# Optimization experiments

Hardware: AMD Instinct MI355X
Metric: run time of the kernel (lower is better)

Reference implementation:

```python
import jax, jax.numpy as jnp
import numpy as np

N, E, H, G, L = 50000, 640000, 128, 8, 3

def setup_inputs() -> dict:
    key = jax.random.key(0)
    ks = jax.random.split(key, 10)
    s = 1.0 / np.sqrt(H)
    return {
        "x": jax.random.normal(ks[0], (N, H), jnp.float32),
        "query": jax.random.normal(ks[1], (G, H), jnp.float32),
        "Wl": jax.random.normal(ks[2], (L, H, H), jnp.float32) * s,
        "bl": jax.random.normal(ks[3], (L, H), jnp.float32) * s,
        "Wr": jax.random.normal(ks[4], (L, H, H), jnp.float32) * s,
        "Wlin": jax.random.normal(ks[5], (H, H), jnp.float32) * s,
        "blin": jax.random.normal(ks[6], (H,), jnp.float32) * s,
        "edge_index": jax.random.randint(ks[7], (2, E), 0, N, jnp.int64),
        "batch_vec": jnp.sort(jax.random.randint(ks[8], (N,), 0, G, jnp.int64)),
    }

def reference(x, query, Wl, bl, Wr, Wlin, blin, edge_index, batch_vec):
    src, dst = edge_index[0], edge_index[1]
    n = x.shape[0]
    for i in range(L):
        # SAGEConv(aggr='max'): gather neighbor feats, scatter-max to dst
        m = jax.ops.segment_max(x[src], dst, num_segments=n)  # [N,H]
        m = jnp.where(jnp.isfinite(m), m, 0.0)  # isolated nodes -> 0 (PyG)
        x = jax.nn.relu(m @ Wl[i].T + bl[i] + x @ Wr[i].T)
    x = x @ Wlin.T + blin  # encoder final linear
    # cosine scoring per graph, vectorized via batch_vec
    xn = x / jnp.linalg.norm(x, axis=1, keepdims=True).clip(1e-12)
    qn = query / jnp.linalg.norm(query, axis=1, keepdims=True).clip(1e-12)
    scores = jnp.sum(xn * qn[batch_vec], axis=1)  # [N]
    return scores
```

## Files before the change

kernel.cpp:

```cpp
#include <hip/hip_runtime.h>
#include <math.h>

#define H 128

typedef _Float16 half8 __attribute__((ext_vector_type(8)));
typedef float f32x16 __attribute__((ext_vector_type(16)));
typedef int int4v __attribute__((ext_vector_type(4)));

__device__ __forceinline__ half8 h8max(half8 a, half8 b) {
#if defined(__has_builtin) && __has_builtin(__builtin_elementwise_max)
    return __builtin_elementwise_max(a, b);
#else
    half8 r;
#pragma unroll
    for (int j = 0; j < 8; ++j) r[j] = a[j] > b[j] ? a[j] : b[j];
    return r;
#endif
}

__device__ __forceinline__ half8 h8shfl_xor(half8 v, int mask) {
    int4v iv;
    __builtin_memcpy(&iv, &v, 16);
#pragma unroll
    for (int j = 0; j < 4; ++j) iv[j] = __shfl_xor(iv[j], mask, 64);
    half8 r;
    __builtin_memcpy(&r, &iv, 16);
    return r;
}


__global__ __launch_bounds__(256) void prep_all(
    const int* __restrict__ ei, int E, int* __restrict__ deg,
    int* __restrict__ govf, int* __restrict__ ovf, int* __restrict__ adjp32,
    const float* __restrict__ x, const float* __restrict__ query,
    const float* __restrict__ Wl, const float* __restrict__ Wr,
    const float* __restrict__ Wlin, _Float16* __restrict__ xh,
    _Float16* __restrict__ wimg, float* __restrict__ qn, int n8, int HB, int SB,
    int WB) {
    int b = blockIdx.x;
    int tid = threadIdx.x;
    if (b < HB) {
        int base = b * 2048 + tid;
        int sv[8], dv[8], posv[8];
#pragma unroll
        for (int k = 0; k < 8; ++k) {
            int e = base + k * 256;
            sv[k] = (e < E) ? ei[e] : 0;
            dv[k] = (e < E) ? ei[E + e] : -1;
        }
#pragma unroll
        for (int k = 0; k < 8; ++k)
            posv[k] = (dv[k] >= 0) ? atomicAdd(&deg[dv[k]], 1) : 0;
#pragma unroll
        for (int k = 0; k < 8; ++k) {
            if (dv[k] >= 0) {
                if (posv[k] < 32) {
                    adjp32[(size_t)dv[k] * 32 + posv[k]] = sv[k];
                } else {
                    int o = atomicAdd(govf, 1);
                    ovf[2 * o] = dv[k];
                    ovf[2 * o + 1] = sv[k];
                }
            }
        }
    } else if (b < HB + SB) {
        int i = (b - HB) * 256 + tid;
        if (i < n8) {
            const float4* x4 = (const float4*)x;
            float4 u = x4[(size_t)i * 2], v = x4[(size_t)i * 2 + 1];
            float f[8] = {u.x, u.y, u.z, u.w, v.x, v.y, v.z, v.w};
            half8 h;
#pragma unroll
            for (int j = 0; j < 8; ++j) h[j] = (_Float16)f[j];
            *(half8*)(xh + (size_t)i * 8) = h;
        }
    } else if (b < HB + SB + WB) {
        int gidx = (b - HB - SB) * 256 + tid;
        if (gidx < 7 * 2048) {
            int mat = gidx / 2048;
            int rem = gidx - mat * 2048;
            int kc4 = rem >> 9;
            int r2 = rem & 511;
            int s = r2 >> 6;
            int lane = r2 & 63;
            int ks = s >> 2;
            int colgrp = s & 3;
            int lhi = lane >> 5, l31 = lane & 31;
            int n = colgrp * 32 + l31;
            int g16 = kc4 * 4 + ks * 2 + lhi;
            const float* src = (mat == 6) ? Wlin
                             : ((mat & 1) ? Wr + (mat >> 1) * H * H
                                          : Wl + (mat >> 1) * H * H);
            const float* p = src + n * H + g16 * 8;
            half8 h, l;
#pragma unroll
            for (int j = 0; j < 8; ++j) {
                float v = p[j];
                _Float16 hh = (_Float16)v;
                h[j] = hh;
                l[j] = (_Float16)(v - (float)hh);
            }
            size_t base = (size_t)mat * 32768 + (size_t)kc4 * 8192 +
                          (size_t)s * 1024 + (size_t)lane * 16;
            *(half8*)(wimg + base) = h;
            *(half8*)(wimg + base + 8) = l;
        }
    } else {
        int g = b - HB - SB - WB;
        __shared__ float part[4];
        float v = (tid < 128) ? query[g * H + tid] : 0.f;
        float ss = v * v;
#pragma unroll
        for (int off = 32; off > 0; off >>= 1) ss += __shfl_xor(ss, off, 64);
        if ((tid & 63) == 0) part[tid >> 6] = ss;
        __syncthreads();
        float tot = part[0] + part[1];
        if (tid < 128) qn[g * H + tid] = v / fmaxf(sqrtf(tot), 1e-12f);
    }
}


template <bool FINAL_UNUSED>
__global__ __launch_bounds__(512, 8) void layer_fused(
    const half8* __restrict__ Xh, const int* __restrict__ deg,
    const int* __restrict__ adjp32, const int* __restrict__ ovf,
    const int* __restrict__ ovfcnt, const _Float16* __restrict__ Bimg,
    const float* __restrict__ bias, _Float16* __restrict__ Yh, int N) {
    __shared__ __align__(16) unsigned char smem[16384];
    _Float16* sU = (_Float16*)smem;
    _Float16* sX = (_Float16*)(smem + 8192);
    float* comb = (float*)smem;

    int tid = threadIdx.x;
    int w = tid >> 6;
    int wq = w & 3;
    int wh = w >> 2;
    int lane = tid & 63;
    int l31 = lane & 31;
    int lhi = lane >> 5;
    int n0 = blockIdx.x * 32;

    const half8 hz = {(_Float16)0.f, (_Float16)0.f, (_Float16)0.f, (_Float16)0.f,
                      (_Float16)0.f, (_Float16)0.f, (_Float16)0.f, (_Float16)0.f};

    {
        int row = tid >> 4;
        int g = tid & 15;
        int nn = n0 + row;
        half8 h = hz;
        if (nn < N) h = Xh[(size_t)nn * 16 + g];
        *(half8*)&sX[row * 128 + ((g ^ (row & 15)) << 3)] = h;
    }

    {
        int sub = lane >> 4;
        int lf = lane & 15;
        int nd4 = n0 + w * 4;
        int node = nd4 + sub;
        int nodec = node < N ? node : N - 1;
        int degv = (node < N) ? deg[node] : 0;

        int dmx = degv;
        {
            int t = __shfl_xor(dmx, 16, 64);
            dmx = t > dmx ? t : dmx;
            t = __shfl_xor(dmx, 32, 64);
            dmx = t > dmx ? t : dmx;
        }

        int r0 = adjp32[(size_t)nodec * 32 + lf];
        int r1 = 0;
        if (dmx > 16) r1 = adjp32[(size_t)nodec * 32 + 16 + lf];
#pragma unroll
        for (int i = 0; i < 4; ++i) {
            int d = __shfl(degv, i << 4, 64);
            int base = i << 4;
            int j0 = sub, j1 = 4 + sub, j2 = 8 + sub, j3 = 12 + sub;
            int i0 = __shfl(r0, base | (j0 < d ? j0 : 0), 64);
            int i1 = __shfl(r0, base | (j1 < d ? j1 : 0), 64);
            int i2 = __shfl(r0, base | (j2 < d ? j2 : 0), 64);
            int i3 = __shfl(r0, base | (j3 < d ? j3 : 0), 64);
            half8 v0 = Xh[(size_t)i0 * 16 + lf];
            half8 v1 = Xh[(size_t)i1 * 16 + lf];
            half8 v2 = Xh[(size_t)i2 * 16 + lf];
            half8 v3 = Xh[(size_t)i3 * 16 + lf];
            half8 acc = h8max(h8max(v0, v1), h8max(v2, v3));
            if (d > 16) {
                int k4 = (16 + sub) < d ? sub : 0;
                int k5 = (20 + sub) < d ? 4 + sub : 0;
                int k6 = (24 + sub) < d ? 8 + sub : 0;
                int k7 = (28 + sub) < d ? 12 + sub : 0;
                int i4 = __shfl(r1, base | k4, 64);
                int i5 = __shfl(r1, base | k5, 64);
                int i6 = __shfl(r1, base | k6, 64);
                int i7 = __shfl(r1, base | k7, 64);
                half8 u0 = Xh[(size_t)i4 * 16 + lf];
                half8 u1 = Xh[(size_t)i5 * 16 + lf];
                half8 u2 = Xh[(size_t)i6 * 16 + lf];
                half8 u3 = Xh[(size_t)i7 * 16 + lf];
                acc = h8max(acc, h8max(h8max(u0, u1), h8max(u2, u3)));
            }
            if (d > 32) {
                int cnt = ovfcnt[0];
                for (int k = 0; k < cnt; ++k) {
                    if (ovf[2 * k] == nd4 + i) {
                        half8 u = Xh[(size_t)ovf[2 * k + 1] * 16 + lf];
                        acc = h8max(acc, u);
                    }
                }
            }
            acc = h8max(acc, h8shfl_xor(acc, 16));
            acc = h8max(acc, h8shfl_xor(acc, 32));
            if (d == 0) acc = hz;
            int row = w * 4 + i;
            if (sub == 0) *(half8*)&sU[row * 128 + ((lf ^ (row & 15)) << 3)] = acc;
        }
    }
    __syncthreads();

    f32x16 acc;
    int col = wq * 32 + l31;
    {
        float b0 = (wh == 0) ? bias[col] : 0.f;
#pragma unroll
        for (int r = 0; r < 16; ++r) acc[r] = b0;
    }

    int rl = l31;
    const _Float16* A = wh ? sX : sU;
    const _Float16* B = Bimg + (size_t)wh * 32768;

#pragma unroll
    for (int kc4 = 0; kc4 < 4; ++kc4) {
#pragma unroll
        for (int ks = 0; ks < 2; ++ks) {
            int g16 = kc4 * 4 + ks * 2 + lhi;
            int posA = g16 ^ (rl & 15);
            half8 ah = *(const half8*)&A[rl * 128 + posA * 8];
            size_t boff =
                (size_t)kc4 * 8192 + (size_t)(ks * 4 + wq) * 1024 + (size_t)lane * 16;
            half8 bh = *(const half8*)&B[boff];
            half8 bl2 = *(const half8*)&B[boff + 8];
            acc = __builtin_amdgcn_mfma_f32_32x32x16_f16(ah, bh, acc, 0, 0, 0);
            acc = __builtin_amdgcn_mfma_f32_32x32x16_f16(ah, bl2, acc, 0, 0, 0);
        }
    }

    __syncthreads();

    if (wh == 1) {
#pragma unroll
        for (int r = 0; r < 16; ++r) {
            int rloc = (r & 3) + 8 * (r >> 2) + 4 * lhi;
            comb[wq * 1024 + rloc * 32 + l31] = acc[r];
        }
    }
    __syncthreads();

    if (wh == 0) {
#pragma unroll
        for (int r = 0; r < 16; ++r) {
            int rloc = (r & 3) + 8 * (r >> 2) + 4 * lhi;
            float y = acc[r] + comb[wq * 1024 + rloc * 32 + l31];
            int row = n0 + rloc;
            if (row < N) Yh[(size_t)row * H + col] = (_Float16)fmaxf(y, 0.f);
        }
    }
}


__global__ __launch_bounds__(256) void final_mfma6(
    const half8* __restrict__ Xh, const _Float16* __restrict__ Bimg,
    const float* __restrict__ blin, const float* __restrict__ qn,
    const int* __restrict__ bv, float* __restrict__ out, int N) {
    __shared__ __align__(16) _Float16 sA[4096];

    int tid = threadIdx.x;
    int w = tid >> 6;
    int lane = tid & 63;
    int l31 = lane & 31;
    int lhi = lane >> 5;
    int n0 = blockIdx.x * 32;

    {
        const half8 hz = {(_Float16)0.f, (_Float16)0.f, (_Float16)0.f, (_Float16)0.f,
                          (_Float16)0.f, (_Float16)0.f, (_Float16)0.f, (_Float16)0.f};
#pragma unroll
        for (int t = 0; t < 2; ++t) {
            int idx = tid + t * 256;
            int row = idx >> 4;
            int g = idx & 15;
            int nn = n0 + row;
            half8 h = hz;
            if (nn < N) h = Xh[(size_t)nn * 16 + g];
            *(half8*)&sA[row * 128 + ((g ^ (row & 15)) << 3)] = h;
        }
    }

    int arow = n0 + l31;
    arow = arow < N ? arow : N - 1;
    int gl = bv[arow];

    f32x16 acc;
    int col = w * 32 + l31;
    {
        float b = blin[col];
#pragma unroll
        for (int r = 0; r < 16; ++r) acc[r] = b;
    }
    int rl = l31;
    __syncthreads();

#pragma unroll
    for (int kc4 = 0; kc4 < 4; ++kc4) {
#pragma unroll
        for (int ks = 0; ks < 2; ++ks) {
            int g16 = kc4 * 4 + ks * 2 + lhi;
            int posA = g16 ^ (rl & 15);
            half8 ah = *(const half8*)&sA[rl * 128 + posA * 8];
            size_t boff =
                (size_t)kc4 * 8192 + (size_t)(ks * 4 + w) * 1024 + (size_t)lane * 16;
            half8 bh = *(const half8*)&Bimg[boff];
            half8 bl2 = *(const half8*)&Bimg[boff + 8];
            acc = __builtin_amdgcn_mfma_f32_32x32x16_f16(ah, bh, acc, 0, 0, 0);
            acc = __builtin_amdgcn_mfma_f32_32x32x16_f16(ah, bl2, acc, 0, 0, 0);
        }
    }

    __syncthreads();
    float* sP = (float*)sA;
#pragma unroll
    for (int r = 0; r < 16; ++r) {
        int rloc = (r & 3) + 8 * (r >> 2) + 4 * lhi;
        int g = __shfl(gl, rloc, 32);
        float y = acc[r];
        float q = qn[(size_t)g * H + col];
        float ss = y * y;
        float sd = y * q;
#pragma unroll
        for (int off = 1; off <= 16; off <<= 1) {
            ss += __shfl_xor(ss, off, 64);
            sd += __shfl_xor(sd, off, 64);
        }
        if (l31 == 0) {
            sP[(rloc * 4 + w) * 2] = ss;
            sP[(rloc * 4 + w) * 2 + 1] = sd;
        }
    }
    __syncthreads();
    if (tid < 32) {
        int row = n0 + tid;
        if (row < N) {
            float ss = 0.f, sd = 0.f;
#pragma unroll
            for (int q = 0; q < 4; ++q) {
                ss += sP[(tid * 4 + q) * 2];
                sd += sP[(tid * 4 + q) * 2 + 1];
            }
            out[row] = sd / fmaxf(sqrtf(ss), 1e-12f);
        }
    }
}


extern "C" void kernel_launch(void* const* d_in, const int* in_sizes, int n_in,
                              void* d_out, int out_size, void* d_ws, size_t ws_size,
                              hipStream_t stream) {
    const float* x = (const float*)d_in[0];
    const float* query = (const float*)d_in[1];
    const float* Wl = (const float*)d_in[2];
    const float* bl = (const float*)d_in[3];
    const float* Wr = (const float*)d_in[4];
    const float* Wlin = (const float*)d_in[5];
    const float* blin = (const float*)d_in[6];
    const int* ei = (const int*)d_in[7];
    const int* bv = (const int*)d_in[8];
    float* out = (float*)d_out;

    const int N = in_sizes[0] / H;
    const int E = in_sizes[7] / 2;
    const int G = in_sizes[1] / H;

    char* p = (char*)d_ws;
    auto alloc = [&](size_t bytes) {
        char* r = p;
        p += (bytes + 255) & ~(size_t)255;
        return r;
    };
    int* deg = (int*)alloc((size_t)(N + 1) * sizeof(int));
    int* govf = deg + N;
    int* adjp32 = (int*)alloc((size_t)N * 32 * sizeof(int));
    int* ovf = (int*)alloc((size_t)E * 2 * sizeof(int));
    float* qn = (float*)alloc((size_t)G * H * sizeof(float));
    _Float16* wimg = (_Float16*)alloc((size_t)7 * 32768 * sizeof(_Float16));
    size_t actH = (size_t)N * H * sizeof(_Float16);
    _Float16* xah = (_Float16*)alloc(actH);
    _Float16* xbh = (_Float16*)alloc(actH);

    hipMemsetAsync(deg, 0, (size_t)(N + 1) * sizeof(int), stream);
    hipMemsetAsync(adjp32, 0, (size_t)N * 32 * sizeof(int), stream);

    const int n8 = N * H / 8;
    const int HB = (E + 2047) / 2048;
    const int SB = (n8 + 255) / 256;
    const int WB = (7 * 2048 + 255) / 256;
    prep_all<<<HB + SB + WB + G, 256, 0, stream>>>(ei, E, deg, govf, ovf,
                                                   adjp32, x, query, Wl, Wr,
                                                   Wlin, xah, wimg, qn, n8, HB,
                                                   SB, WB);

    const int NGm = (N + 31) / 32;

    layer_fused<false><<<NGm, 512, 0, stream>>>(
        (const half8*)xah, deg, adjp32, ovf, govf, wimg + (size_t)0 * 65536,
        bl + 0 * H, xbh, N);
    layer_fused<false><<<NGm, 512, 0, stream>>>(
        (const half8*)xbh, deg, adjp32, ovf, govf, wimg + (size_t)1 * 65536,
        bl + 1 * H, xah, N);
    layer_fused<false><<<NGm, 512, 0, stream>>>(
        (const half8*)xah, deg, adjp32, ovf, govf, wimg + (size_t)2 * 65536,
        bl + 2 * H, xbh, N);
    final_mfma6<<<NGm, 256, 0, stream>>>(
        (const half8*)xbh, wimg + (size_t)6 * 32768, blin, qn, bv, out, N);
}
```

Before: 246.6 us.

## Build padded adjacency via two-pass bucket sort instead of global atomics

Replaces the global-atomic adjacency build with a counting sort. Each block histograms destination buckets of 256 nodes, the edges are scattered into bucket order, and one block per bucket then assembles the padded 32-slot rows in shared memory and writes them out coalesced. This removes the random global atomics on deg and the scattered 4-byte adjacency writes, and it drops the two large memsets. In exchange it adds two kernel launches, a serial prefix scan over HB per bucket in every scatter block, and an extra E×8-byte intermediate buffer.

```diff
diff --git a/kernel.cpp b/kernel.cpp
--- a/kernel.cpp
+++ b/kernel.cpp
@@ -2,6 +2,7 @@
 #include <math.h>
 
 #define H 128
+#define NBUCK_MAX 256
 
 typedef _Float16 half8 __attribute__((ext_vector_type(8)));
 typedef float f32x16 __attribute__((ext_vector_type(16)));
@@ -30,8 +31,7 @@
 
 
 __global__ __launch_bounds__(256) void prep_all(
-    const int* __restrict__ ei, int E, int* __restrict__ deg,
-    int* __restrict__ govf, int* __restrict__ ovf, int* __restrict__ adjp32,
+    const int* __restrict__ ei, int E, int* __restrict__ blockhist, int NB,
     const float* __restrict__ x, const float* __restrict__ query,
     const float* __restrict__ Wl, const float* __restrict__ Wr,
     const float* __restrict__ Wlin, _Float16* __restrict__ xh,
@@ -40,29 +40,17 @@
     int b = blockIdx.x;
     int tid = threadIdx.x;
     if (b < HB) {
+        __shared__ int hist[NBUCK_MAX];
+        for (int j = tid; j < NB; j += 256) hist[j] = 0;
+        __syncthreads();
         int base = b * 2048 + tid;
-        int sv[8], dv[8], posv[8];
 #pragma unroll
         for (int k = 0; k < 8; ++k) {
             int e = base + k * 256;
-            sv[k] = (e < E) ? ei[e] : 0;
-            dv[k] = (e < E) ? ei[E + e] : -1;
-        }
-#pragma unroll
-        for (int k = 0; k < 8; ++k)
-            posv[k] = (dv[k] >= 0) ? atomicAdd(&deg[dv[k]], 1) : 0;
-#pragma unroll
-        for (int k = 0; k < 8; ++k) {
-            if (dv[k] >= 0) {
-                if (posv[k] < 32) {
-                    adjp32[(size_t)dv[k] * 32 + posv[k]] = sv[k];
-                } else {
-                    int o = atomicAdd(govf, 1);
-                    ovf[2 * o] = dv[k];
-                    ovf[2 * o + 1] = sv[k];
-                }
-            }
-        }
+            if (e < E) atomicAdd(&hist[ei[E + e] >> 8], 1);
+        }
+        __syncthreads();
+        for (int j = tid; j < NB; j += 256) blockhist[(size_t)b * NB + j] = hist[j];
     } else if (b < HB + SB) {
         int i = (b - HB) * 256 + tid;
         if (i < n8) {
@@ -116,6 +104,105 @@
         __syncthreads();
         float tot = part[0] + part[1];
         if (tid < 128) qn[g * H + tid] = v / fmaxf(sqrtf(tot), 1e-12f);
+    }
+}
+
+
+__global__ __launch_bounds__(256) void scatter_edges(
+    const int* __restrict__ ei, int E, const int* __restrict__ blockhist,
+    int HB, int NB, int2* __restrict__ bucketed, int* __restrict__ colstart,
+    int* __restrict__ coltot) {
+    __shared__ int sbase[NBUCK_MAX];
+    __shared__ int stot[NBUCK_MAX];
+    __shared__ int scnt[NBUCK_MAX];
+    int b = blockIdx.x;
+    int tid = threadIdx.x;
+
+    for (int j = tid; j < NB; j += 256) {
+        int off = 0, tot = 0;
+        for (int bb = 0; bb < HB; ++bb) {
+            int v = blockhist[(size_t)bb * NB + j];
+            off += (bb < b) ? v : 0;
+            tot += v;
+        }
+        sbase[j] = off;
+        stot[j] = tot;
+        scnt[j] = 0;
+    }
+    __syncthreads();
+    if (tid == 0) {
+        int run = 0;
+        for (int j = 0; j < NB; ++j) {
+            int t = stot[j];
+            stot[j] = run;
+            run += t;
+        }
+    }
+    __syncthreads();
+    for (int j = tid; j < NB; j += 256) {
+        sbase[j] += stot[j];
+        if (b == 0) {
+            colstart[j] = stot[j];
+        }
+    }
+    __syncthreads();
+    if (b == 0) {
+        for (int j = tid; j < NB; j += 256) {
+            int tot = 0;
+            for (int bb = 0; bb < HB; ++bb) tot += blockhist[(size_t)bb * NB + j];
+            coltot[j] = tot;
+        }
+    }
+    int base = b * 2048 + tid;
+#pragma unroll
+    for (int k = 0; k < 8; ++k) {
+        int e = base + k * 256;
+        if (e < E) {
+            int s = ei[e];
+            int d = ei[E + e];
+            int bu = d >> 8;
+            int r = atomicAdd(&scnt[bu], 1);
+            bucketed[sbase[bu] + r] = make_int2(d, s);
+        }
+    }
+}
+
+
+__global__ __launch_bounds__(256) void build_rows(
+    const int2* __restrict__ bucketed, const int* __restrict__ colstart,
+    const int* __restrict__ coltot, int* __restrict__ deg,
+    int* __restrict__ adjp32, int* __restrict__ govf, int* __restrict__ ovf,
+    int N) {
+    __shared__ __align__(16) int rows[256 * 32];
+    __shared__ int cnt[256];
+    int k = blockIdx.x;
+    int tid = threadIdx.x;
+    cnt[tid] = 0;
+    for (int j = tid; j < 256 * 32; j += 256) rows[j] = 0;
+    __syncthreads();
+
+    int s0 = colstart[k];
+    int cn = coltot[k];
+    for (int i = tid; i < cn; i += 256) {
+        int2 rec = bucketed[s0 + i];
+        int dl = rec.x & 255;
+        int sl = atomicAdd(&cnt[dl], 1);
+        if (sl < 32) {
+            rows[dl * 32 + sl] = rec.y;
+        } else {
+            int o = atomicAdd(govf, 1);
+            ovf[2 * o] = rec.x;
+            ovf[2 * o + 1] = rec.y;
+        }
+    }
+    __syncthreads();
+    int node0 = k << 8;
+    if (node0 + tid < N) deg[node0 + tid] = cnt[tid];
+    for (int j = tid; j < 2048; j += 256) {
+        int row = j >> 3, q = j & 7;
+        int node = node0 + row;
+        if (node < N)
+            ((int4*)adjp32)[(size_t)node * 8 + q] = ((const int4*)rows)[row * 8 + q];
     }
 }
 
@@ -201,10 +288,10 @@
                 acc = h8max(acc, h8max(h8max(u0, u1), h8max(u2, u3)));
             }
             if (d > 32) {
-                int cnt = ovfcnt[0];
-                for (int k = 0; k < cnt; ++k) {
-                    if (ovf[2 * k] == nd4 + i) {
-                        half8 u = Xh[(size_t)ovf[2 * k + 1] * 16 + lf];
+                int cntv = ovfcnt[0];
+                for (int kk = 0; kk < cntv; ++kk) {
+                    if (ovf[2 * kk] == nd4 + i) {
+                        half8 u = Xh[(size_t)ovf[2 * kk + 1] * 16 + lf];
                         acc = h8max(acc, u);
                     }
                 }
@@ -381,6 +468,9 @@
     const int E = in_sizes[7] / 2;
     const int G = in_sizes[1] / H;
 
+    const int HB = (E + 2047) / 2048;
+    const int NB = (N + 255) >> 8;
+
     char* p = (char*)d_ws;
     auto alloc = [&](size_t bytes) {
         char* r = p;
@@ -391,23 +481,28 @@
     int* govf = deg + N;
     int* adjp32 = (int*)alloc((size_t)N * 32 * sizeof(int));
     int* ovf = (int*)alloc((size_t)E * 2 * sizeof(int));
+    int* blockhist = (int*)alloc((size_t)HB * NB * sizeof(int));
+    int* colstart = (int*)alloc((size_t)NB * sizeof(int));
+    int* coltot = (int*)alloc((size_t)NB * sizeof(int));
+    int2* bucketed = (int2*)alloc((size_t)E * sizeof(int2));
     float* qn = (float*)alloc((size_t)G * H * sizeof(float));
     _Float16* wimg = (_Float16*)alloc((size_t)7 * 32768 * sizeof(_Float16));
     size_t actH = (size_t)N * H * sizeof(_Float16);
     _Float16* xah = (_Float16*)alloc(actH);
     _Float16* xbh = (_Float16*)alloc(actH);
 
-    hipMemsetAsync(deg, 0, (size_t)(N + 1) * sizeof(int), stream);
-    hipMemsetAsync(adjp32, 0, (size_t)N * 32 * sizeof(int), stream);
+    hipMemsetAsync(govf, 0, sizeof(int), stream);
 
     const int n8 = N * H / 8;
-    const int HB = (E + 2047) / 2048;
     const int SB = (n8 + 255) / 256;
     const int WB = (7 * 2048 + 255) / 256;
-    prep_all<<<HB + SB + WB + G, 256, 0, stream>>>(ei, E, deg, govf, ovf,
-                                                   adjp32, x, query, Wl, Wr,
-                                                   Wlin, xah, wimg, qn, n8, HB,
-                                                   SB, WB);
+    prep_all<<<HB + SB + WB + G, 256, 0, stream>>>(ei, E, blockhist, NB, x,
+                                                   query, Wl, Wr, Wlin, xah,
+                                                   wimg, qn, n8, HB, SB, WB);
+    scatter_edges<<<HB, 256, 0, stream>>>(ei, E, blockhist, HB, NB, bucketed,
+                                          colstart, coltot);
+    build_rows<<<NB, 256, 0, stream>>>(bucketed, colstart, coltot, deg, adjp32,
+                                       govf, ovf, N);
 
     const int NGm = (N + 31) / 32;
 
```

After: 331.3 us. 1.34x slower.
